# Optimization experiments

Hardware: AMD Instinct MI355X
Metric: run time of the kernel (lower is better)

The kernel has to match this reference:

```python
import jax, jax.numpy as jnp
import numpy as np

N_LAYERS = 2
N_COEF = 5
IN_DIM = 256
LN_EPS = 1e-6  # flax LayerNorm default


def jacobi_design(x, a, n):
    """Jacobi polynomials P_0..P_{n-1}^{(a,a)}(x). x: [...], returns [..., n]."""
    Ps = [jnp.ones_like(x)]
    if n > 1:
        Ps.append((a + 1.0) * x)
    for k in range(2, n):
        t = 2.0 * k + 2.0 * a
        A = 2.0 * k * (k + 2.0 * a) * (t - 2.0)
        B = (t - 1.0) * t * (t - 2.0)
        C = 2.0 * (k + a - 1.0) ** 2 * t
        Ps.append((B * x * Ps[-1] - C * Ps[-2]) / A)
    return jnp.stack(Ps, axis=-1)


def setup_inputs() -> dict:
    key = jax.random.key(0)
    k1, k2 = jax.random.split(key)
    x = jax.random.normal(k1, (8192, IN_DIM), dtype=jnp.float32)
    coefs = jax.random.normal(k2, (N_LAYERS, IN_DIM, IN_DIM, N_COEF), dtype=jnp.float32) * 0.03
    alphas = jnp.zeros((N_LAYERS,), dtype=jnp.float32)      # alpha_arctanh init zeros
    ln_scale = jnp.ones((N_LAYERS, IN_DIM), dtype=jnp.float32)
    ln_bias = jnp.zeros((N_LAYERS, IN_DIM), dtype=jnp.float32)
    return {"x": x, "coefs": coefs, "alphas": alphas, "ln_scale": ln_scale, "ln_bias": ln_bias}


def reference(x, coefs, alphas, ln_scale, ln_bias):
    h = x  # [B, D]
    for l in range(N_LAYERS):
        # LayerNorm
        mu = jnp.mean(h, axis=-1, keepdims=True)
        var = jnp.mean(jnp.square(h - mu), axis=-1, keepdims=True)
        hn = (h - mu) * jax.lax.rsqrt(var + LN_EPS) * ln_scale[l] + ln_bias[l]
        # KANLayer: Jacobi design matrix on tanh-mapped input
        a = jnp.tanh(alphas[l])
        dm = jacobi_design(jnp.tanh(hn), a, N_COEF)  # [B, D, C]
        # resid_scale=0, spline_scale=1, dropout inactive -> y = mean_i einsum
        in_dim = hn.shape[-1]
        h = jnp.einsum('bic,ioc->bo', dm, coefs[l]) / in_dim  # [B, D]
    return h
```

## Files before the change

kernel.cpp:

```cpp
#include <hip/hip_runtime.h>

#define D 256
#define NB 8192
#define NKC 128
#define PANEL (NKC * 512)

#define SXX_STRIDE 264
#define SXX_ELEMS (32 * SXX_STRIDE)
#define WREG 4096
#define SMEM_BYTES (SXX_ELEMS * 2 + 8 * WREG * 2)

typedef __bf16 bf16;
typedef bf16 bf16x8 __attribute__((ext_vector_type(8)));
typedef bf16 bf16x4 __attribute__((ext_vector_type(4)));
typedef float f32x4 __attribute__((ext_vector_type(4)));

__device__ __forceinline__ float fast_tanh(float x) {
    float e = __expf(2.f * x);
    return 1.f - 2.f / (e + 1.f);
}

__global__ __launch_bounds__(256) void pack_kernel(const float* __restrict__ coefs,
                                                   bf16* __restrict__ Wt,
                                                   float* __restrict__ beta) {
    __shared__ float t[64 * 65];
    __shared__ float accs[4][64];
    int b = blockIdx.x;
    if (b < 128) {
        int l = b >> 6, rem = b & 63;
        int c = (rem >> 4) + 1, tl = rem & 15;
        int plane = (c == 1) ? 0 : (c == 4) ? 1 : (c == 2) ? 2 : 3;
        int i0 = (tl >> 2) * 64, o0 = (tl & 3) * 64;

        for (int j = threadIdx.x; j < 4096; j += 256) {
            int i = j >> 6, o = j & 63;
            t[i * 65 + o] = coefs[(((size_t)(l * 256 + i0 + i)) * 256 + (o0 + o)) * 5 + c];
        }
        __syncthreads();
        bf16* dst = Wt + (size_t)l * (4 * PANEL)
                       + ((size_t)(tl & 3) * NKC + (plane * 256 + i0) / 8) * 512;
        for (int j = threadIdx.x; j < 4096; j += 256) {
            int il = j & 7, o = (j >> 3) & 63, ih = j >> 9;
            dst[j] = (bf16)t[(ih * 8 + il) * 65 + o];
        }
    } else {
        int lidx = b - 128;
        int l = lidx >> 2, o0 = (lidx & 3) * 64;
        int o = threadIdx.x & 63, ig = threadIdx.x >> 6;
        float sum = 0.f;
        for (int m = 0; m < 64; ++m) {
            int i = ig * 64 + m;
            sum += coefs[(((size_t)(l * 256 + i)) * 256 + (o0 + o)) * 5 + 0];
        }
        accs[ig][o] = sum;
        __syncthreads();
        if (threadIdx.x < 64)
            beta[l * 256 + o0 + threadIdx.x] = accs[0][threadIdx.x] + accs[1][threadIdx.x]
                                             + accs[2][threadIdx.x] + accs[3][threadIdx.x];
    }
}

#define CHOFF(PH, it) (((((PH) * 2 + ((it) & 1)) * 8) + ((it) >> 1)) * 2048)

template <int PH>
__device__ __forceinline__ void gemm_half(f32x4 (&acc)[2][4], bf16x8 (&wf)[4][4],
                                          const bf16* __restrict__ lane,
                                          const bf16* sxx, int l, float a1,
                                          float rB0, float rB1, float rB2,
                                          float rC0, float rC1, float rC2) {
    bf16x8 afn[2];
#pragma unroll
    for (int it = 0; it < 16; ++it) {
        if (it < 14) {
            const int s = (it + 2) & 3;
#pragma unroll
            for (int tn = 0; tn < 4; ++tn)
                wf[s][tn] = *(const bf16x8*)(lane + CHOFF(PH, it + 2) + tn * 128);
        }

        bf16x8 af[2];
        if ((it & 1) == 0) {
            const int j  = it >> 1;
            const int i0 = j * 32 + (l >> 4) * 8;
#pragma unroll
            for (int tm = 0; tm < 2; ++tm) {
                bf16x8 xv = *(const bf16x8*)(sxx + (16 * tm + (l & 15)) * SXX_STRIDE + i0);
#pragma unroll
                for (int jj = 0; jj < 8; ++jj) {
                    float x  = (float)xv[jj];
                    float P1 = a1 * x;
                    float P2 = rB0 * x * P1 - rC0;
                    float P3 = rB1 * x * P2 - rC1 * P1;
                    float PA, PB;
                    if (PH == 0) { PA = P1; PB = rB2 * x * P3 - rC2 * P2; }
                    else         { PA = P2; PB = P3; }
                    af[tm][jj]  = (bf16)PA;
                    afn[tm][jj] = (bf16)PB;
                }
            }
        } else {
            af[0] = afn[0];
            af[1] = afn[1];
        }

        const int cur = it & 3;
#pragma unroll
        for (int tm = 0; tm < 2; ++tm)
#pragma unroll
            for (int tn = 0; tn < 4; ++tn)
                acc[tm][tn] = __builtin_amdgcn_mfma_f32_16x16x32_bf16(
                    af[tm], wf[cur][tn], acc[tm][tn], 0, 0, 0);
    }
}

__global__ __launch_bounds__(512, 2) void fused2_kernel(
    const float* __restrict__ x, const float* __restrict__ ln_scale,
    const float* __restrict__ ln_bias, const float* __restrict__ alphas,
    const bf16* __restrict__ Wt, const float* __restrict__ beta,
    float* __restrict__ out) {
    extern __shared__ __align__(16) bf16 smem[];
    bf16* sxx  = smem;
    bf16* stag = smem + SXX_ELEMS;

    const int tid = threadIdx.x;
    const int l   = tid & 63;
    const int w   = tid >> 6;
    const int g   = w >> 1, p = w & 1;
    const int slab = blockIdx.x;

#pragma unroll
    for (int L = 0; L < 2; ++L) {
        const float* scale = ln_scale + L * D;
        const float* biasp = ln_bias + L * D;
        const bf16*  Wl    = Wt + (size_t)L * 4 * PANEL;
        const float* bet   = beta + L * D;

        const bf16* lane = Wl + (size_t)g * PANEL + (l >> 4) * 512 + (l & 15) * 8;

        bf16x8 wf[4][4];
#pragma unroll
        for (int s = 0; s < 2; ++s)
#pragma unroll
            for (int tn = 0; tn < 4; ++tn)
                wf[s][tn] = *(const bf16x8*)(lane + (p * 16 + s * 8) * 2048 + tn * 128);

        const float a  = tanhf(alphas[L]);
        const float a1 = a + 1.f;
        float rB[3], rC[3];
#pragma unroll
        for (int k = 2; k < 5; k++) {
            float tk  = 2.f * k + 2.f * a;
            float iAk = 1.f / (2.f * k * (k + 2.f * a) * (tk - 2.f));
            rB[k - 2] = (tk - 1.f) * tk * (tk - 2.f) * iAk;
            rC[k - 2] = 2.f * (k + a - 1.f) * (k + a - 1.f) * tk * iAk;
        }

        float4 sc4 = ((const float4*)scale)[l];
        float4 bi4 = ((const float4*)biasp)[l];
        float scv[4] = {sc4.x, sc4.y, sc4.z, sc4.w};
        float biv[4] = {bi4.x, bi4.y, bi4.z, bi4.w};

#pragma unroll
        for (int rr = 0; rr < 4; ++rr) {
            int lr = w * 4 + rr;
            float4 v;
            if (L == 0) {
                v = ((const float4*)(x + ((size_t)slab * 32 + lr) * D))[l];
            } else {
                const float* hp = (const float*)(stag + (size_t)(l >> 4) * 2 * WREG);
                v = *(const float4*)(hp + lr * 64 + (l & 15) * 4);
            }
            float s  = v.x + v.y + v.z + v.w;
            float ss = v.x * v.x + v.y * v.y + v.z * v.z + v.w * v.w;
#pragma unroll
            for (int off = 32; off > 0; off >>= 1) {
                s  += __shfl_down(s, off);
                ss += __shfl_down(ss, off);
            }
            s  = __shfl(s, 0);
            ss = __shfl(ss, 0);
            float mu   = s * (1.f / D);
            float rstd = rsqrtf(ss * (1.f / D) - mu * mu + 1e-6f);
            float hv[4] = {v.x, v.y, v.z, v.w};
            bf16x4 o;
#pragma unroll
            for (int e = 0; e < 4; ++e)
                o[e] = (bf16)fast_tanh((hv[e] - mu) * rstd * scv[e] + biv[e]);
            *(bf16x4*)(sxx + lr * SXX_STRIDE + 4 * l) = o;
        }
        __syncthreads();

        f32x4 acc[2][4] = {};
        if (p == 0) gemm_half<0>(acc, wf, lane, sxx, l, a1, rB[0], rB[1], rB[2], rC[0], rC[1], rC[2]);
        else        gemm_half<1>(acc, wf, lane, sxx, l, a1, rB[0], rB[1], rB[2], rC[0], rC[1], rC[2]);

        if (p == 1) {
            f32x4* dumpr = (f32x4*)(stag + (size_t)w * WREG);
#pragma unroll
            for (int tm = 0; tm < 2; ++tm)
#pragma unroll
                for (int tn = 0; tn < 4; ++tn)
                    dumpr[(tm * 4 + tn) * 64 + l] = acc[tm][tn];
        }
        __syncthreads();

        if (p == 0) {
            f32x4* part = (f32x4*)(stag + (size_t)(w + 1) * WREG);
            if (L == 0) {
                float* hp = (float*)(stag + (size_t)w * WREG);
#pragma unroll
                for (int tm = 0; tm < 2; ++tm)
#pragma unroll
                    for (int tn = 0; tn < 4; ++tn) {
                        int lc = 16 * tn + (l & 15);
                        float bv = bet[g * 64 + lc] * (1.f / 256.f);
                        f32x4 v = acc[tm][tn] + part[(tm * 4 + tn) * 64 + l];
                        int lr0 = 16 * tm + (l >> 4) * 4;
#pragma unroll
                        for (int r = 0; r < 4; ++r)
                            hp[(lr0 + r) * 64 + lc] = v[r] * (1.f / 256.f) + bv;
                    }
            } else {
#pragma unroll
                for (int tm = 0; tm < 2; ++tm)
#pragma unroll
                    for (int tn = 0; tn < 4; ++tn) {
                        int gc = g * 64 + 16 * tn + (l & 15);
                        float bv = bet[gc] * (1.f / 256.f);
                        f32x4 v = acc[tm][tn] + part[(tm * 4 + tn) * 64 + l];
                        int gr = slab * 32 + 16 * tm + (l >> 4) * 4;
#pragma unroll
                        for (int r = 0; r < 4; ++r)
                            out[(size_t)(gr + r) * D + gc] = v[r] * (1.f / 256.f) + bv;
                    }
            }
        }
        __syncthreads();
    }
}

extern "C" void kernel_launch(void* const* d_in, const int* in_sizes, int n_in,
                              void* d_out, int out_size, void* d_ws, size_t ws_size,
                              hipStream_t stream) {
    const float* x        = (const float*)d_in[0];
    const float* coefs    = (const float*)d_in[1];
    const float* alphas   = (const float*)d_in[2];
    const float* ln_scale = (const float*)d_in[3];
    const float* ln_bias  = (const float*)d_in[4];
    float* out = (float*)d_out;

    char* ws = (char*)d_ws;
    bf16*  Wt   = (bf16*)ws;
    float* beta = (float*)(ws + 1048576);

    hipFuncSetAttribute((const void*)fused2_kernel,
                        hipFuncAttributeMaxDynamicSharedMemorySize, SMEM_BYTES);

    pack_kernel<<<136, 256, 0, stream>>>(coefs, Wt, beta);
    fused2_kernel<<<256, 512, SMEM_BYTES, stream>>>(x, ln_scale, ln_bias, alphas,
                                                    Wt, beta, out);
}
```

Measured before the change: 93.79 us.

## Split output columns across waves instead of K, removing cross-wave reduction

Each of the 8 waves now computes a 32-column output slice over the full K (all four polynomial planes) instead of pairs of waves splitting K and reducing partial sums through shared memory. This removes the partial-sum dump, one barrier and the add pass, and shrinks the staging LDS, which now uses a padded stride. In exchange, each wave computes all Jacobi terms for every tile (the polynomial work is duplicated across more waves) and holds fewer accumulators with a 3-deep weight prefetch ring. The pack layout is simplified to planes in natural order.

Result: slower. 96.51 us (+2.9%).

```diff
diff --git a/kernel.cpp b/kernel.cpp
--- a/kernel.cpp
+++ b/kernel.cpp
@@ -7,8 +7,8 @@
 
 #define SXX_STRIDE 264
 #define SXX_ELEMS (32 * SXX_STRIDE)
-#define WREG 4096
-#define SMEM_BYTES (SXX_ELEMS * 2 + 8 * WREG * 2)
+#define H1_STRIDE 36
+#define H1_REGION 1152
 
 typedef __bf16 bf16;
 typedef bf16 bf16x8 __attribute__((ext_vector_type(8)));
@@ -29,7 +29,7 @@
     if (b < 128) {
         int l = b >> 6, rem = b & 63;
         int c = (rem >> 4) + 1, tl = rem & 15;
-        int plane = (c == 1) ? 0 : (c == 4) ? 1 : (c == 2) ? 2 : 3;
+        int plane = c - 1;
         int i0 = (tl >> 2) * 64, o0 = (tl & 3) * 64;
 
         for (int j = threadIdx.x; j < 4096; j += 256) {
@@ -60,72 +60,17 @@
     }
 }
 
-#define CHOFF(PH, it) (((((PH) * 2 + ((it) & 1)) * 8) + ((it) >> 1)) * 2048)
-
-template <int PH>
-__device__ __forceinline__ void gemm_half(f32x4 (&acc)[2][4], bf16x8 (&wf)[4][4],
-                                          const bf16* __restrict__ lane,
-                                          const bf16* sxx, int l, float a1,
-                                          float rB0, float rB1, float rB2,
-                                          float rC0, float rC1, float rC2) {
-    bf16x8 afn[2];
-#pragma unroll
-    for (int it = 0; it < 16; ++it) {
-        if (it < 14) {
-            const int s = (it + 2) & 3;
-#pragma unroll
-            for (int tn = 0; tn < 4; ++tn)
-                wf[s][tn] = *(const bf16x8*)(lane + CHOFF(PH, it + 2) + tn * 128);
-        }
-
-        bf16x8 af[2];
-        if ((it & 1) == 0) {
-            const int j  = it >> 1;
-            const int i0 = j * 32 + (l >> 4) * 8;
-#pragma unroll
-            for (int tm = 0; tm < 2; ++tm) {
-                bf16x8 xv = *(const bf16x8*)(sxx + (16 * tm + (l & 15)) * SXX_STRIDE + i0);
-#pragma unroll
-                for (int jj = 0; jj < 8; ++jj) {
-                    float x  = (float)xv[jj];
-                    float P1 = a1 * x;
-                    float P2 = rB0 * x * P1 - rC0;
-                    float P3 = rB1 * x * P2 - rC1 * P1;
-                    float PA, PB;
-                    if (PH == 0) { PA = P1; PB = rB2 * x * P3 - rC2 * P2; }
-                    else         { PA = P2; PB = P3; }
-                    af[tm][jj]  = (bf16)PA;
-                    afn[tm][jj] = (bf16)PB;
-                }
-            }
-        } else {
-            af[0] = afn[0];
-            af[1] = afn[1];
-        }
-
-        const int cur = it & 3;
-#pragma unroll
-        for (int tm = 0; tm < 2; ++tm)
-#pragma unroll
-            for (int tn = 0; tn < 4; ++tn)
-                acc[tm][tn] = __builtin_amdgcn_mfma_f32_16x16x32_bf16(
-                    af[tm], wf[cur][tn], acc[tm][tn], 0, 0, 0);
-    }
-}
-
 __global__ __launch_bounds__(512, 2) void fused2_kernel(
     const float* __restrict__ x, const float* __restrict__ ln_scale,
     const float* __restrict__ ln_bias, const float* __restrict__ alphas,
     const bf16* __restrict__ Wt, const float* __restrict__ beta,
     float* __restrict__ out) {
-    extern __shared__ __align__(16) bf16 smem[];
-    bf16* sxx  = smem;
-    bf16* stag = smem + SXX_ELEMS;
+    __shared__ __align__(16) bf16 sxx[SXX_ELEMS];
+    __shared__ __align__(16) float stagf[8 * H1_REGION];
 
     const int tid = threadIdx.x;
     const int l   = tid & 63;
     const int w   = tid >> 6;
-    const int g   = w >> 1, p = w & 1;
     const int slab = blockIdx.x;
 
 #pragma unroll
@@ -135,14 +80,15 @@
         const bf16*  Wl    = Wt + (size_t)L * 4 * PANEL;
         const float* bet   = beta + L * D;
 
-        const bf16* lane = Wl + (size_t)g * PANEL + (l >> 4) * 512 + (l & 15) * 8;
-
-        bf16x8 wf[4][4];
+        const bf16* lane = Wl + (size_t)(w >> 1) * PANEL + (l >> 4) * 512
+                              + ((w & 1) * 32 + (l & 15)) * 8;
+
+        bf16x8 wf[3][2];
 #pragma unroll
         for (int s = 0; s < 2; ++s)
 #pragma unroll
-            for (int tn = 0; tn < 4; ++tn)
-                wf[s][tn] = *(const bf16x8*)(lane + (p * 16 + s * 8) * 2048 + tn * 128);
+            for (int tn = 0; tn < 2; ++tn)
+                wf[s][tn] = *(const bf16x8*)(lane + (s * 32) * 512 + tn * 128);
 
         const float a  = tanhf(alphas[L]);
         const float a1 = a + 1.f;
@@ -167,8 +113,8 @@
             if (L == 0) {
                 v = ((const float4*)(x + ((size_t)slab * 32 + lr) * D))[l];
             } else {
-                const float* hp = (const float*)(stag + (size_t)(l >> 4) * 2 * WREG);
-                v = *(const float4*)(hp + lr * 64 + (l & 15) * 4);
+                v = *(const float4*)(stagf + (l >> 3) * H1_REGION + lr * H1_STRIDE
+                                     + 4 * (l & 7));
             }
             float s  = v.x + v.y + v.z + v.w;
             float ss = v.x * v.x + v.y * v.y + v.z * v.z + v.w * v.w;
@@ -190,50 +136,81 @@
         }
         __syncthreads();
 
-        f32x4 acc[2][4] = {};
-        if (p == 0) gemm_half<0>(acc, wf, lane, sxx, l, a1, rB[0], rB[1], rB[2], rC[0], rC[1], rC[2]);
-        else        gemm_half<1>(acc, wf, lane, sxx, l, a1, rB[0], rB[1], rB[2], rC[0], rC[1], rC[2]);
-
-        if (p == 1) {
-            f32x4* dumpr = (f32x4*)(stag + (size_t)w * WREG);
+        f32x4 acc[2][2] = {};
+        bf16x8 pc2[2], pc3[2], pc4[2];
+#pragma unroll
+        for (int j = 0; j < 8; ++j) {
+#pragma unroll
+            for (int q = 0; q < 4; ++q) {
+                const int it = j * 4 + q;
+                if (it < 30) {
+                    const int itp = it + 2;
+                    const int jp = itp >> 2, qp = itp & 3;
+                    const int s = itp % 3;
+#pragma unroll
+                    for (int tn = 0; tn < 2; ++tn)
+                        wf[s][tn] = *(const bf16x8*)(lane + (qp * 32 + jp * 4) * 512
+                                                     + tn * 128);
+                }
+
+                bf16x8 af[2];
+                if (q == 0) {
+                    const int i0 = j * 32 + (l >> 4) * 8;
+#pragma unroll
+                    for (int tm = 0; tm < 2; ++tm) {
+                        bf16x8 xv = *(const bf16x8*)(sxx + (16 * tm + (l & 15)) * SXX_STRIDE + i0);
+#pragma unroll
+                        for (int jj = 0; jj < 8; ++jj) {
+                            float xx = (float)xv[jj];
+                            float P1 = a1 * xx;
+                            float P2 = rB[0] * xx * P1 - rC[0];
+                            float P3 = rB[1] * xx * P2 - rC[1] * P1;
+                            float P4 = rB[2] * xx * P3 - rC[2] * P2;
+                            af[tm][jj]  = (bf16)P1;
+                            pc2[tm][jj] = (bf16)P2;
+                            pc3[tm][jj] = (bf16)P3;
+                            pc4[tm][jj] = (bf16)P4;
+                        }
+                    }
+                } else if (q == 1) { af[0] = pc2[0]; af[1] = pc2[1]; }
+                else if (q == 2)   { af[0] = pc3[0]; af[1] = pc3[1]; }
+                else               { af[0] = pc4[0]; af[1] = pc4[1]; }
+
+                const int cur = it % 3;
+#pragma unroll
+                for (int tm = 0; tm < 2; ++tm)
+#pragma unroll
+                    for (int tn = 0; tn < 2; ++tn)
+                        acc[tm][tn] = __builtin_amdgcn_mfma_f32_16x16x32_bf16(
+                            af[tm], wf[cur][tn], acc[tm][tn], 0, 0, 0);
+            }
+        }
+
+        if (L == 0) {
+            float* hp = stagf + w * H1_REGION;
 #pragma unroll
             for (int tm = 0; tm < 2; ++tm)
 #pragma unroll
-                for (int tn = 0; tn < 4; ++tn)
-                    dumpr[(tm * 4 + tn) * 64 + l] = acc[tm][tn];
-        }
-        __syncthreads();
-
-        if (p == 0) {
-            f32x4* part = (f32x4*)(stag + (size_t)(w + 1) * WREG);
-            if (L == 0) {
-                float* hp = (float*)(stag + (size_t)w * WREG);
-#pragma unroll
-                for (int tm = 0; tm < 2; ++tm)
-#pragma unroll
-                    for (int tn = 0; tn < 4; ++tn) {
-                        int lc = 16 * tn + (l & 15);
-                        float bv = bet[g * 64 + lc] * (1.f / 256.f);
-                        f32x4 v = acc[tm][tn] + part[(tm * 4 + tn) * 64 + l];
-                        int lr0 = 16 * tm + (l >> 4) * 4;
-#pragma unroll
-                        for (int r = 0; r < 4; ++r)
-                            hp[(lr0 + r) * 64 + lc] = v[r] * (1.f / 256.f) + bv;
-                    }
-            } else {
-#pragma unroll
-                for (int tm = 0; tm < 2; ++tm)
-#pragma unroll
-                    for (int tn = 0; tn < 4; ++tn) {
-                        int gc = g * 64 + 16 * tn + (l & 15);
-                        float bv = bet[gc] * (1.f / 256.f);
-                        f32x4 v = acc[tm][tn] + part[(tm * 4 + tn) * 64 + l];
-                        int gr = slab * 32 + 16 * tm + (l >> 4) * 4;
-#pragma unroll
-                        for (int r = 0; r < 4; ++r)
-                            out[(size_t)(gr + r) * D + gc] = v[r] * (1.f / 256.f) + bv;
-                    }
-            }
+                for (int tn = 0; tn < 2; ++tn) {
+                    int lc = tn * 16 + (l & 15);
+                    float bv = bet[w * 32 + lc] * (1.f / 256.f);
+                    int lr0 = tm * 16 + (l >> 4) * 4;
+#pragma unroll
+                    for (int r = 0; r < 4; ++r)
+                        hp[(lr0 + r) * H1_STRIDE + lc] = acc[tm][tn][r] * (1.f / 256.f) + bv;
+                }
+        } else {
+#pragma unroll
+            for (int tm = 0; tm < 2; ++tm)
+#pragma unroll
+                for (int tn = 0; tn < 2; ++tn) {
+                    int gc = w * 32 + tn * 16 + (l & 15);
+                    float bv = bet[gc] * (1.f / 256.f);
+                    int gr = slab * 32 + tm * 16 + (l >> 4) * 4;
+#pragma unroll
+                    for (int r = 0; r < 4; ++r)
+                        out[(size_t)(gr + r) * D + gc] = acc[tm][tn][r] * (1.f / 256.f) + bv;
+                }
         }
         __syncthreads();
     }
@@ -253,10 +230,6 @@
     bf16*  Wt   = (bf16*)ws;
     float* beta = (float*)(ws + 1048576);
 
-    hipFuncSetAttribute((const void*)fused2_kernel,
-                        hipFuncAttributeMaxDynamicSharedMemorySize, SMEM_BYTES);
-
     pack_kernel<<<136, 256, 0, stream>>>(coefs, Wt, beta);
-    fused2_kernel<<<256, 512, SMEM_BYTES, stream>>>(x, ln_scale, ln_bias, alphas,
-                                                    Wt, beta, out);
-}
+    fused2_kernel<<<256, 512, 0, stream>>>(x, ln_scale, ln_bias, alphas, Wt, beta, out);
+}
```
